# Performance work log

Hardware: AMD Instinct MI355X
Metric: run time of the kernel (lower is better)

## Reference

```python
import jax, jax.numpy as jnp
import numpy as np

BETA = 0.9
GAMMA = -0.1
EPSILON = 1.1
EPS = 1e-08

NUM_INPUTS = 8
NUM_OUTPUTS = 8
UNITS = 256
BATCH = 8192


def setup_inputs() -> dict:
    key = jax.random.key(0)
    k_x, k_a, k_u, k_t = jax.random.split(key, 4)
    x_stack = jax.random.normal(k_x, (BATCH, NUM_INPUTS, UNITS), dtype=jnp.float32)
    alpha = jax.random.uniform(k_a, (1,), dtype=jnp.float32)  # torch.rand(1)
    u_param = jax.random.uniform(k_u, (NUM_OUTPUTS, NUM_INPUTS), dtype=jnp.float32,
                                 minval=EPS, maxval=1.0 - EPS)
    # xavier_normal_ on [o, n, u, u]: fan_in = n*u*u? torch: fan_out = o*u*u, fan_in = n*u*u
    fan_in = NUM_INPUTS * UNITS * UNITS
    fan_out = NUM_OUTPUTS * UNITS * UNITS
    std = float(np.sqrt(2.0 / (fan_in + fan_out)))
    trans_matrix = std * jax.random.normal(k_t, (NUM_OUTPUTS, NUM_INPUTS, UNITS, UNITS),
                                           dtype=jnp.float32)
    return {"x_stack": x_stack, "alpha": alpha, "u_param": u_param,
            "trans_matrix": trans_matrix}


def reference(x_stack, alpha, u_param, trans_matrix):
    # Hard-concrete style gate: s = sigmoid(logit(u) + log(alpha)/beta)
    s = jax.nn.sigmoid(jnp.log(u_param) - jnp.log(1.0 - u_param)
                       + jnp.log(alpha) / BETA)          # [o, n]
    z = jnp.clip(s * (EPSILON - GAMMA) + GAMMA, 0.0, 1.0)  # [o, n]
    # Fused gated grouped matmul + reduction over inputs n:
    # equivalent to einsum('bnu,onuv->bonv') * z[None,:,:,None] summed over n.
    out = jnp.einsum('bnu,onuv,on->bov', x_stack, trans_matrix, z)  # [b, o, v]
    return out
```

## Files before the change

kernel.cpp:

```cpp
#include <hip/hip_runtime.h>
#include <hip/hip_bf16.h>

#define BATCH 8192
#define KDIM  2048
#define NDIM  2048
#define BM 128
#define BN 128
#define BK 32

typedef short bf16x8 __attribute__((ext_vector_type(8)));
typedef float f32x4  __attribute__((ext_vector_type(4)));

__device__ __forceinline__ unsigned short f2bf(float f) {
    unsigned int u = __float_as_uint(f);
    u = u + 0x7fffu + ((u >> 16) & 1u);
    return (unsigned short)(u >> 16);
}

__global__ __launch_bounds__(256) void pack_a(const float* __restrict__ x,
                                              short* __restrict__ a) {
    int h = blockIdx.x * 256 + threadIdx.x;
    const f32x4* xv = (const f32x4*)x;
    f32x4 v0 = xv[(size_t)h * 2];
    f32x4 v1 = xv[(size_t)h * 2 + 1];
    bf16x8 r;
    r[0] = (short)f2bf(v0[0]); r[1] = (short)f2bf(v0[1]);
    r[2] = (short)f2bf(v0[2]); r[3] = (short)f2bf(v0[3]);
    r[4] = (short)f2bf(v1[0]); r[5] = (short)f2bf(v1[1]);
    r[6] = (short)f2bf(v1[2]); r[7] = (short)f2bf(v1[3]);
    ((bf16x8*)a)[h] = r;
}

__global__ __launch_bounds__(256) void pack_b(const float* __restrict__ T,
                                              const float* __restrict__ u_param,
                                              const float* __restrict__ alpha,
                                              short* __restrict__ bp) {
    int g = blockIdx.x * 256 + threadIdx.x;
    int j = g >> 8, c = g & 255;
    int o = j >> 8, v = j & 255;
    int n = c >> 5, u0 = (c & 31) * 8;
    float up = u_param[o * 8 + n];
    float t  = logf(up) - logf(1.0f - up) + logf(alpha[0]) * (1.0f / 0.9f);
    float s  = 1.0f / (1.0f + expf(-t));
    float z  = s * 1.2f - 0.1f;
    z = fminf(fmaxf(z, 0.0f), 1.0f);
    const float* tp = T + (((size_t)(o * 8 + n)) << 16) + (size_t)u0 * 256 + v;
    bf16x8 r;
#pragma unroll
    for (int i = 0; i < 8; ++i) r[i] = (short)f2bf(z * tp[(size_t)i * 256]);
    ((bf16x8*)bp)[(size_t)j * 256 + c] = r;
}

__global__ __launch_bounds__(256, 2) void gemm(const short* __restrict__ A,
                                               const short* __restrict__ B,
                                               float* __restrict__ C) {
    __shared__ __align__(16) short As[2][BM * BK];
    __shared__ __align__(16) short Bs[2][BN * BK];

    int tid = threadIdx.x;
    int bid = blockIdx.x;
    int wg = (bid & 7) * 128 + (bid >> 3);
    int bx = wg & 15, by = wg >> 4;
    int bm = by * BM, bn = bx * BN;

    int wid = tid >> 6, lane = tid & 63;
    int wr = wid >> 1, wc = wid & 1;
    int lrow = lane & 15, lk = lane >> 4;

    f32x4 acc[4][4] = {};

    auto stage = [&](int buf, int kt) {
#pragma unroll
        for (int i = 0; i < 2; ++i) {
            int c = i * 256 + tid;
            int r = c >> 2, cw = c & 3;
            const short* ga = A + (size_t)(bm + r) * KDIM + kt * BK + cw * 8;
            __builtin_amdgcn_global_load_lds(
                (const __attribute__((address_space(1))) void*)ga,
                (__attribute__((address_space(3))) void*)&As[buf][c * 8], 16, 0, 0);
            const short* gb = B + (size_t)(bn + r) * KDIM + kt * BK + cw * 8;
            __builtin_amdgcn_global_load_lds(
                (const __attribute__((address_space(1))) void*)gb,
                (__attribute__((address_space(3))) void*)&Bs[buf][c * 8], 16, 0, 0);
        }
    };

    stage(0, 0);
    __syncthreads();
    int cur = 0;
    const int NT = KDIM / BK;
    for (int kt = 0; kt < NT; ++kt) {
        if (kt + 1 < NT) stage(cur ^ 1, kt + 1);
        bf16x8 a[4], b[4];
#pragma unroll
        for (int m = 0; m < 4; ++m)
            a[m] = *(const bf16x8*)&As[cur][(wr * 64 + m * 16 + lrow) * BK + lk * 8];
#pragma unroll
        for (int n = 0; n < 4; ++n)
            b[n] = *(const bf16x8*)&Bs[cur][(wc * 64 + n * 16 + lrow) * BK + lk * 8];
#pragma unroll
        for (int m = 0; m < 4; ++m)
#pragma unroll
            for (int n = 0; n < 4; ++n)
                acc[m][n] = __builtin_amdgcn_mfma_f32_16x16x32_bf16(a[m], b[n], acc[m][n], 0, 0, 0);
        __syncthreads();
        cur ^= 1;
    }

    int r0 = bm + wr * 64 + (lane >> 4) * 4;
    int c0 = bn + wc * 64 + lrow;
#pragma unroll
    for (int m = 0; m < 4; ++m)
#pragma unroll
        for (int n = 0; n < 4; ++n)
#pragma unroll
            for (int r = 0; r < 4; ++r)
                C[(size_t)(r0 + m * 16 + r) * NDIM + (c0 + n * 16)] = acc[m][n][r];
}

extern "C" void kernel_launch(void* const* d_in, const int* in_sizes, int n_in,
                              void* d_out, int out_size, void* d_ws, size_t ws_size,
                              hipStream_t stream) {
    const float* x       = (const float*)d_in[0];
    const float* alpha   = (const float*)d_in[1];
    const float* u_param = (const float*)d_in[2];
    const float* T       = (const float*)d_in[3];
    float* out = (float*)d_out;

    short* Abf = (short*)d_ws;
    short* Bp  = (short*)((char*)d_ws + (size_t)BATCH * KDIM * 2);

    hipLaunchKernelGGL(pack_a, dim3((BATCH * KDIM / 8) / 256), dim3(256), 0, stream, x, Abf);
    hipLaunchKernelGGL(pack_b, dim3((NDIM * KDIM / 8) / 256), dim3(256), 0, stream,
                       T, u_param, alpha, Bp);
    hipLaunchKernelGGL(gemm, dim3((BATCH / BM) * (NDIM / BN)), dim3(256), 0, stream,
                       Abf, Bp, out);
}
```

Measured before the change: 227.3 us.

## Rewrite GEMM with 256x256 tiles, swizzled LDS, interleaved pipeline; tile-transpose pack_b

The GEMM moves from 128x128x32 tiles with 4 waves to 256x256x64 tiles with 8 waves, using an XOR-swizzled LDS layout to avoid bank conflicts. The main loop interleaves LDS reads, async global-to-LDS stages and MFMA quarters, separated by explicit sched/s_barriers, with setprio around the MFMAs. pack_b now transposes through a padded shared-memory tile so its global reads and writes are coalesced. The larger tiles raise register and LDS use per block, and the hand-scheduled waitcnt ordering is fragile.

```diff
diff --git a/kernel.cpp b/kernel.cpp
--- a/kernel.cpp
+++ b/kernel.cpp
@@ -4,9 +4,6 @@
 #define BATCH 8192
 #define KDIM  2048
 #define NDIM  2048
-#define BM 128
-#define BN 128
-#define BK 32
 
 typedef short bf16x8 __attribute__((ext_vector_type(8)));
 typedef float f32x4  __attribute__((ext_vector_type(4)));
@@ -35,87 +32,161 @@
                                               const float* __restrict__ u_param,
                                               const float* __restrict__ alpha,
                                               short* __restrict__ bp) {
-    int g = blockIdx.x * 256 + threadIdx.x;
-    int j = g >> 8, c = g & 255;
-    int o = j >> 8, v = j & 255;
-    int n = c >> 5, u0 = (c & 31) * 8;
+    __shared__ short tl[256 * 33];
+    int bid = blockIdx.x;
+    int o  = bid >> 6;
+    int n  = (bid >> 3) & 7;
+    int v0 = (bid & 7) * 32;
+    int tid = threadIdx.x;
+
     float up = u_param[o * 8 + n];
     float t  = logf(up) - logf(1.0f - up) + logf(alpha[0]) * (1.0f / 0.9f);
     float s  = 1.0f / (1.0f + expf(-t));
-    float z  = s * 1.2f - 0.1f;
-    z = fminf(fmaxf(z, 0.0f), 1.0f);
-    const float* tp = T + (((size_t)(o * 8 + n)) << 16) + (size_t)u0 * 256 + v;
-    bf16x8 r;
-#pragma unroll
-    for (int i = 0; i < 8; ++i) r[i] = (short)f2bf(z * tp[(size_t)i * 256]);
-    ((bf16x8*)bp)[(size_t)j * 256 + c] = r;
-}
-
-__global__ __launch_bounds__(256, 2) void gemm(const short* __restrict__ A,
+    float z  = fminf(fmaxf(s * 1.2f - 0.1f, 0.0f), 1.0f);
+
+    const f32x4* T4 = (const f32x4*)(T + ((size_t)(o * 8 + n) << 16));
+#pragma unroll
+    for (int it = 0; it < 8; ++it) {
+        int f = it * 256 + tid;
+        int u = f >> 3, vv = (f & 7) * 4;
+        f32x4 val = T4[(u * 256 + v0 + vv) >> 2];
+#pragma unroll
+        for (int j = 0; j < 4; ++j)
+            tl[u * 33 + vv + j] = (short)f2bf(z * val[j]);
+    }
+    __syncthreads();
+#pragma unroll
+    for (int it = 0; it < 4; ++it) {
+        int g = it * 256 + tid;
+        int v = g >> 5, ch = g & 31;
+        bf16x8 r;
+#pragma unroll
+        for (int q = 0; q < 8; ++q) r[q] = tl[(ch * 8 + q) * 33 + v];
+        *(bf16x8*)&bp[(size_t)(o * 256 + v0 + v) * KDIM + n * 256 + ch * 8] = r;
+    }
+}
+
+#define SBAR() do { __builtin_amdgcn_sched_barrier(0); \
+                    __builtin_amdgcn_s_barrier(); \
+                    __builtin_amdgcn_sched_barrier(0); } while (0)
+
+#define MMQ(q) do { \
+    __builtin_amdgcn_s_setprio(1); \
+    _Pragma("unroll") for (int mm = 0; mm < 2; ++mm) \
+    _Pragma("unroll") for (int nn = 0; nn < 4; ++nn) \
+    _Pragma("unroll") for (int k8 = 0; k8 < 2; ++k8) \
+        acc[(q)*2 + mm][nn] = __builtin_amdgcn_mfma_f32_16x16x32_bf16( \
+            afr[mm][k8], bfr[nn][k8], acc[(q)*2 + mm][nn], 0, 0, 0); \
+    __builtin_amdgcn_s_setprio(0); \
+} while (0)
+
+__global__ __launch_bounds__(512, 2) void gemm(const short* __restrict__ A,
                                                const short* __restrict__ B,
                                                float* __restrict__ C) {
-    __shared__ __align__(16) short As[2][BM * BK];
-    __shared__ __align__(16) short Bs[2][BN * BK];
-
-    int tid = threadIdx.x;
+    __shared__ __align__(16) short lds[65536];
+
+    const int tid  = threadIdx.x;
+    const int lane = tid & 63;
+    const int wid  = tid >> 6;
+    const int wr = wid >> 2, wc = wid & 3;
+    const int l15 = lane & 15, hi8 = (lane >> 4) * 8;
+    const int sx  = ((lane >> 2) & 1) << 4;
+
     int bid = blockIdx.x;
-    int wg = (bid & 7) * 128 + (bid >> 3);
-    int bx = wg & 15, by = wg >> 4;
-    int bm = by * BM, bn = bx * BN;
-
-    int wid = tid >> 6, lane = tid & 63;
-    int wr = wid >> 1, wc = wid & 1;
-    int lrow = lane & 15, lk = lane >> 4;
-
-    f32x4 acc[4][4] = {};
-
-    auto stage = [&](int buf, int kt) {
+    int wg  = (bid & 7) * 32 + (bid >> 3);
+    int by = wg >> 3, bx = wg & 7;
+    const int bm = by * 256, bn = bx * 256;
+
+    int r_[2], c_[2];
+#pragma unroll
+    for (int i = 0; i < 2; ++i) {
+        int L = i * 4096 + tid * 8;
+        int S = L ^ (((L >> 8) & 1) << 4);
+        r_[i] = S >> 6; c_[i] = S & 63;
+    }
+
+    auto stA = [&](int buf, int h, int kt) {
 #pragma unroll
         for (int i = 0; i < 2; ++i) {
-            int c = i * 256 + tid;
-            int r = c >> 2, cw = c & 3;
-            const short* ga = A + (size_t)(bm + r) * KDIM + kt * BK + cw * 8;
+            const short* src = A + (size_t)(bm + h * 128 + r_[i]) * KDIM + kt * 64 + c_[i];
             __builtin_amdgcn_global_load_lds(
-                (const __attribute__((address_space(1))) void*)ga,
-                (__attribute__((address_space(3))) void*)&As[buf][c * 8], 16, 0, 0);
-            const short* gb = B + (size_t)(bn + r) * KDIM + kt * BK + cw * 8;
+                (const __attribute__((address_space(1))) void*)src,
+                (__attribute__((address_space(3))) void*)&lds[buf * 16384 + h * 8192 + i * 4096 + tid * 8],
+                16, 0, 0);
+        }
+    };
+    auto stB = [&](int buf, int h, int kt) {
+#pragma unroll
+        for (int i = 0; i < 2; ++i) {
+            const short* src = B + (size_t)(bn + h * 128 + r_[i]) * KDIM + kt * 64 + c_[i];
             __builtin_amdgcn_global_load_lds(
-                (const __attribute__((address_space(1))) void*)gb,
-                (__attribute__((address_space(3))) void*)&Bs[buf][c * 8], 16, 0, 0);
+                (const __attribute__((address_space(1))) void*)src,
+                (__attribute__((address_space(3))) void*)&lds[32768 + buf * 16384 + h * 8192 + i * 4096 + tid * 8],
+                16, 0, 0);
         }
     };
 
-    stage(0, 0);
-    __syncthreads();
-    int cur = 0;
-    const int NT = KDIM / BK;
-    for (int kt = 0; kt < NT; ++kt) {
-        if (kt + 1 < NT) stage(cur ^ 1, kt + 1);
-        bf16x8 a[4], b[4];
-#pragma unroll
-        for (int m = 0; m < 4; ++m)
-            a[m] = *(const bf16x8*)&As[cur][(wr * 64 + m * 16 + lrow) * BK + lk * 8];
-#pragma unroll
-        for (int n = 0; n < 4; ++n)
-            b[n] = *(const bf16x8*)&Bs[cur][(wc * 64 + n * 16 + lrow) * BK + lk * 8];
-#pragma unroll
-        for (int m = 0; m < 4; ++m)
-#pragma unroll
-            for (int n = 0; n < 4; ++n)
-                acc[m][n] = __builtin_amdgcn_mfma_f32_16x16x32_bf16(a[m], b[n], acc[m][n], 0, 0, 0);
-        __syncthreads();
-        cur ^= 1;
-    }
-
-    int r0 = bm + wr * 64 + (lane >> 4) * 4;
-    int c0 = bn + wc * 64 + lrow;
-#pragma unroll
-    for (int m = 0; m < 4; ++m)
-#pragma unroll
-        for (int n = 0; n < 4; ++n)
+    f32x4  acc[8][4] = {};
+    bf16x8 bfr[4][2];
+    bf16x8 afr[2][2];
+
+    auto rdB = [&](int buf) {
+        int base = 32768 + buf * 16384 + (wc * 64 + l15) * 64 + hi8;
+#pragma unroll
+        for (int nn = 0; nn < 4; ++nn)
+#pragma unroll
+            for (int k8 = 0; k8 < 2; ++k8)
+                bfr[nn][k8] = *(const bf16x8*)&lds[(base + nn * 1024 + k8 * 32) ^ sx];
+    };
+    auto rdA = [&](int buf, int q) {
+        int base = buf * 16384 + (wr * 128 + q * 32 + l15) * 64 + hi8;
+#pragma unroll
+        for (int mm = 0; mm < 2; ++mm)
+#pragma unroll
+            for (int k8 = 0; k8 < 2; ++k8)
+                afr[mm][k8] = *(const bf16x8*)&lds[(base + mm * 1024 + k8 * 32) ^ sx];
+    };
+
+    stA(0, 0, 0); stA(0, 1, 0);
+    stB(0, 0, 0); stB(0, 1, 0);
+    stB(1, 0, 1); stB(1, 1, 1);
+    asm volatile("s_waitcnt vmcnt(4)" ::: "memory");
+    SBAR();
+
+    for (int i = 0; i < 16; ++i) {
+        int t1 = 2 * i + 1, t2 = (2 * i + 2) & 31, t3 = (2 * i + 3) & 31;
+        rdB(0); rdA(0, 0); stA(1, 0, t1);
+        SBAR(); MMQ(0); SBAR();
+        rdA(0, 1); stA(1, 1, t1);
+        SBAR(); MMQ(1); SBAR();
+        rdA(0, 2); stB(0, 0, t2);
+        SBAR(); MMQ(2); SBAR();
+        rdA(0, 3); stB(0, 1, t2);
+        SBAR(); MMQ(3);
+        asm volatile("s_waitcnt vmcnt(4)" ::: "memory");
+        SBAR();
+        rdB(1); rdA(1, 0); stA(0, 0, t2);
+        SBAR(); MMQ(0); SBAR();
+        rdA(1, 1); stA(0, 1, t2);
+        SBAR(); MMQ(1); SBAR();
+        rdA(1, 2); stB(1, 0, t3);
+        SBAR(); MMQ(2); SBAR();
+        rdA(1, 3); stB(1, 1, t3);
+        SBAR(); MMQ(3);
+        asm volatile("s_waitcnt vmcnt(4)" ::: "memory");
+        SBAR();
+    }
+    asm volatile("s_waitcnt vmcnt(0)" ::: "memory");
+
+    int r0 = bm + wr * 128 + (lane >> 4) * 4;
+    int c0 = bn + wc * 64 + l15;
+#pragma unroll
+    for (int m = 0; m < 8; ++m)
+#pragma unroll
+        for (int nn = 0; nn < 4; ++nn)
 #pragma unroll
             for (int r = 0; r < 4; ++r)
-                C[(size_t)(r0 + m * 16 + r) * NDIM + (c0 + n * 16)] = acc[m][n][r];
+                C[(size_t)(r0 + m * 16 + r) * NDIM + c0 + nn * 16] = acc[m][nn][r];
 }
 
 extern "C" void kernel_launch(void* const* d_in, const int* in_sizes, int n_in,
@@ -131,8 +202,7 @@
     short* Bp  = (short*)((char*)d_ws + (size_t)BATCH * KDIM * 2);
 
     hipLaunchKernelGGL(pack_a, dim3((BATCH * KDIM / 8) / 256), dim3(256), 0, stream, x, Abf);
-    hipLaunchKernelGGL(pack_b, dim3((NDIM * KDIM / 8) / 256), dim3(256), 0, stream,
-                       T, u_param, alpha, Bp);
-    hipLaunchKernelGGL(gemm, dim3((BATCH / BM) * (NDIM / BN)), dim3(256), 0, stream,
+    hipLaunchKernelGGL(pack_b, dim3(512), dim3(256), 0, stream, T, u_param, alpha, Bp);
+    hipLaunchKernelGGL(gemm, dim3((BATCH / 256) * (NDIM / 256)), dim3(512), 0, stream,
                        Abf, Bp, out);
 }
```

Measured after the change: 193.2 us. 1.18x faster.
